# Kernel optimization log

Measured on AMD Instinct MI355X. Metric: run time of the kernel, lower is better.

Reference implementation:

```python
import jax, jax.numpy as jnp
import numpy as np

SHIFT = 1  # fixed shift_direction (original picks +-1 randomly at init)


def setup_inputs() -> dict:
    key = jax.random.key(0)
    kx, kw = jax.random.split(key)
    x = jax.random.normal(kx, (128, 256, 28, 28), dtype=jnp.float32)
    W = jax.random.normal(kw, (32, 3, 4, 3, 8), dtype=jnp.float32)
    return {"x": x, "W": W}


def reference(x, W):
    # (128,256,28,28) -> (128,2,128,28,28) -> sum over dim 1 -> (128,128,28,28)
    t = x.reshape(128, 2, 128, 28, 28).sum(axis=1)
    # split channels into 32 groups of 4: (n, i=32, m=4, h=28, w=28)
    t = t.reshape(128, 32, 4, 28, 28)
    # first unfold: kernel (3,1), pad (1,0) over the i=32 axis -> neighbor stack j in {-1,0,+1}
    tp = jnp.pad(t, ((0, 0), (1, 1), (0, 0), (0, 0), (0, 0)))
    t3 = jnp.stack([tp[:, 0:32], tp[:, 1:33], tp[:, 2:34]], axis=1)  # (n, j3, i32, m, h, w)
    # cyclic shift along w
    t3 = jnp.roll(t3, SHIFT, axis=5)
    # second unfold: kernel (3,1), pad (1,0) over the w axis -> neighbor stack kw in {-1,0,+1}
    tp2 = jnp.pad(t3, ((0, 0), (0, 0), (0, 0), (0, 0), (0, 0), (1, 1)))
    t3 = jnp.stack([tp2[..., 0:28], tp2[..., 1:29], tp2[..., 2:30]], axis=5)  # (n, j3, i32, m, h, kw, w)
    # contraction: einsum labels match torch 'njimpol,jimlk->njpok' after its permute.
    # Our t3 dims (n, i_e=3, j_e=32, m=4, p=h, l=kw, o=w); W dims (j=32, i=3, m=4, l=3, k=8)
    out = jnp.einsum('nijmplo,jimlk->njpok', t3, W)  # (128, 32, 28, 28, 8)
    out = out.transpose(0, 2, 3, 1, 4).reshape(128, 28, 28, 256)
    out = jnp.roll(out, SHIFT, axis=1)
    return out.transpose(0, 3, 1, 2)  # (128, 256, 28, 28)
```

## Files before the change

### kernel.cpp

```cpp
#include <hip/hip_runtime.h>

typedef float __attribute__((ext_vector_type(4))) f32x4;
typedef unsigned int u32;
typedef u32 __attribute__((ext_vector_type(4))) u32x4;


__device__ __forceinline__ u32 pack2bf(float lo, float hi) {
    u32 a = __float_as_uint(lo), b = __float_as_uint(hi);
    a = (a + 0x7FFFu + ((a >> 16) & 1u)) >> 16;
    b = (b + 0x7FFFu + ((b >> 16) & 1u)) >> 16;
    return a | (b << 16);
}

__device__ __forceinline__ float dot2bf(u32 t2, u32 w2, float acc) {
    asm("v_dot2_f32_bf16 %0, %1, %2, %0" : "+v"(acc) : "v"(t2), "v"(w2));
    return acc;
}

__global__ __launch_bounds__(256, 8) void fused_shift_conv(
    const float* __restrict__ x, const float* __restrict__ Wt, float* __restrict__ out)
{
    __shared__ __align__(16) u32 L[3840];

    const int tid  = threadIdx.x;
    const int blk  = blockIdx.x;
    const int half = blk & 1;
    const int rest = blk >> 1;
    const int n    = rest / 14;
    const int b2   = rest - n * 14;
    const int h0   = b2 * 2;
    const int J0   = half * 16;

    const float* xn = x + (size_t)n * 200704;

    #pragma unroll
    for (int it = 0; it < 2; ++it) {
        const int f = tid + it * 256;
        if (f < 504) {
            const int pl  = f / 14;
            const int rem = f - pl * 14;
            const int row = rem / 7;
            const int q   = rem - row * 7;
            const int gl  = pl >> 1;
            const int mp  = pl & 1;
            const int g   = J0 - 1 + gl;
            int hs = h0 - 1 + row;
            hs = hs < 0 ? 27 : hs;
            u32x4 wv = {0u, 0u, 0u, 0u};
            if (g >= 0 && g <= 31) {
                const int ch0 = g * 4 + mp * 2;
                const float* b0 = xn + ch0 * 784 + hs * 28 + q * 4;
                const f32x4 l0 = *(const f32x4*)b0;
                const f32x4 l1 = *(const f32x4*)(b0 + 784);
                const f32x4 u0 = *(const f32x4*)(b0 + 100352);
                const f32x4 u1 = *(const f32x4*)(b0 + 784 + 100352);
                const f32x4 s0 = l0 + u0, s1 = l1 + u1;
                #pragma unroll
                for (int e = 0; e < 4; ++e) wv[e] = pack2bf(s0[e], s1[e]);
            }
            const int sw = gl & 7;
            *(u32x4*)&L[row * 1152 + pl * 32 + ((q ^ sw) << 2)] = wv;
        }
    }

    const int tloc = tid & 127;
    const int s_   = tid >> 7;
    const int jl   = tloc >> 3;
    const int j    = J0 + jl;
    const int k    = tloc & 7;
    u32 w2[3][2][3];
    {
        const float* wp = Wt + j * 288 + k;
        #pragma unroll
        for (int a = 0; a < 3; ++a)
            #pragma unroll
            for (int m2 = 0; m2 < 2; ++m2)
                #pragma unroll
                for (int bb = 0; bb < 3; ++bb)
                    w2[a][m2][bb] = pack2bf(wp[a*96 + (2*m2  )*24 + bb*8],
                                            wp[a*96 + (2*m2+1)*24 + bb*8]);
    }
    if (j == 0) {
        #pragma unroll
        for (int m2 = 0; m2 < 2; ++m2)
            #pragma unroll
            for (int bb = 0; bb < 3; ++bb) w2[0][m2][bb] = 0u;
    }
    if (j == 31) {
        #pragma unroll
        for (int m2 = 0; m2 < 2; ++m2)
            #pragma unroll
            for (int bb = 0; bb < 3; ++bb) w2[2][m2][bb] = 0u;
    }

    int rb_c[4], rb_r[4];
    #pragma unroll
    for (int it = 0; it < 4; ++it) {
        const int fo = tid + it * 256;
        rb_c[it] = fo / 14;
        rb_r[it] = fo - rb_c[it] * 14;
    }

    __syncthreads();

    const u32* Bs = L + s_ * 1152;
    float acc[28];
    #pragma unroll
    for (int w = 0; w < 28; ++w) acc[w] = 0.f;

    #pragma unroll
    for (int a = 0; a < 3; ++a) {
        const int gl = jl + a;
        const int s  = gl & 7;
        #pragma unroll
        for (int m2 = 0; m2 < 2; ++m2) {
            const int rowd = (gl * 2 + m2) * 32;
            const u32 t2 = w2[a][m2][2], t1 = w2[a][m2][1], t0 = w2[a][m2][0];
            #pragma unroll
            for (int qb = 0; qb < 7; ++qb) {
                const u32x4 v = *(const u32x4*)&Bs[rowd + ((qb ^ s) << 2)];
                #pragma unroll
                for (int e = 0; e < 4; ++e) {
                    const int wp_ = qb * 4 + e;
                    if (wp_ != 27) acc[wp_] = dot2bf(v[e], t2, acc[wp_]);
                    acc[(wp_ + 1) % 28] = dot2bf(v[e], t1, acc[(wp_ + 1) % 28]);
                    if (wp_ != 26) acc[(wp_ + 2) % 28] = dot2bf(v[e], t0, acc[(wp_ + 2) % 28]);
                }
            }
        }
    }

    float* Lf = (float*)L;
    float* outb = out + (size_t)n * 200704 + (size_t)(J0 * 8) * 784 + h0 * 28;
    #pragma unroll
    for (int c = 0; c < 2; ++c) {
        __syncthreads();
        if ((tloc >> 6) == c) {
            float* dst = Lf + (tloc & 63) * 60 + s_ * 28;
            #pragma unroll
            for (int qq = 0; qq < 7; ++qq) {
                f32x4 o;
                o.x = acc[qq * 4 + 0];
                o.y = acc[qq * 4 + 1];
                o.z = acc[qq * 4 + 2];
                o.w = acc[qq * 4 + 3];
                *(f32x4*)(dst + qq * 4) = o;
            }
        }
        __syncthreads();
        float* outc = outb + (size_t)(c * 64) * 784;
        #pragma unroll
        for (int it = 0; it < 4; ++it) {
            if (tid + it * 256 < 896) {
                const f32x4 v = *(const f32x4*)(Lf + rb_c[it] * 60 + rb_r[it] * 4);
                *(f32x4*)(outc + (size_t)rb_c[it] * 784 + rb_r[it] * 4) = v;
            }
        }
    }
}

extern "C" void kernel_launch(void* const* d_in, const int* in_sizes, int n_in,
                              void* d_out, int out_size, void* d_ws, size_t ws_size,
                              hipStream_t stream) {
    const float* x  = (const float*)d_in[0];
    const float* Wt = (const float*)d_in[1];
    float* out      = (float*)d_out;

    const int nbatch = in_sizes[0] / 200704;
    fused_shift_conv<<<nbatch * 28, 256, 0, stream>>>(x, Wt, out);
}
```

Measured before the change: 50.37 us.

## Process four output rows per block with prefetch of next input rows

Each block now covers four output rows (two passes of two) instead of two, so the grid is halved. The weight packing and index setup are reused across both passes. The second pass's global loads are issued before the first pass's output store so they overlap it. Input and transpose staging now use separate shared buffers, which raises LDS use, and launch bounds drop to 6 blocks per CU, which may reduce occupancy.

```diff
diff --git a/kernel.cpp b/kernel.cpp
--- a/kernel.cpp
+++ b/kernel.cpp
@@ -17,97 +17,10 @@
     return acc;
 }
 
-__global__ __launch_bounds__(256, 8) void fused_shift_conv(
-    const float* __restrict__ x, const float* __restrict__ Wt, float* __restrict__ out)
-{
-    __shared__ __align__(16) u32 L[3840];
-
-    const int tid  = threadIdx.x;
-    const int blk  = blockIdx.x;
-    const int half = blk & 1;
-    const int rest = blk >> 1;
-    const int n    = rest / 14;
-    const int b2   = rest - n * 14;
-    const int h0   = b2 * 2;
-    const int J0   = half * 16;
-
-    const float* xn = x + (size_t)n * 200704;
-
-    #pragma unroll
-    for (int it = 0; it < 2; ++it) {
-        const int f = tid + it * 256;
-        if (f < 504) {
-            const int pl  = f / 14;
-            const int rem = f - pl * 14;
-            const int row = rem / 7;
-            const int q   = rem - row * 7;
-            const int gl  = pl >> 1;
-            const int mp  = pl & 1;
-            const int g   = J0 - 1 + gl;
-            int hs = h0 - 1 + row;
-            hs = hs < 0 ? 27 : hs;
-            u32x4 wv = {0u, 0u, 0u, 0u};
-            if (g >= 0 && g <= 31) {
-                const int ch0 = g * 4 + mp * 2;
-                const float* b0 = xn + ch0 * 784 + hs * 28 + q * 4;
-                const f32x4 l0 = *(const f32x4*)b0;
-                const f32x4 l1 = *(const f32x4*)(b0 + 784);
-                const f32x4 u0 = *(const f32x4*)(b0 + 100352);
-                const f32x4 u1 = *(const f32x4*)(b0 + 784 + 100352);
-                const f32x4 s0 = l0 + u0, s1 = l1 + u1;
-                #pragma unroll
-                for (int e = 0; e < 4; ++e) wv[e] = pack2bf(s0[e], s1[e]);
-            }
-            const int sw = gl & 7;
-            *(u32x4*)&L[row * 1152 + pl * 32 + ((q ^ sw) << 2)] = wv;
-        }
-    }
-
-    const int tloc = tid & 127;
-    const int s_   = tid >> 7;
-    const int jl   = tloc >> 3;
-    const int j    = J0 + jl;
-    const int k    = tloc & 7;
-    u32 w2[3][2][3];
-    {
-        const float* wp = Wt + j * 288 + k;
-        #pragma unroll
-        for (int a = 0; a < 3; ++a)
-            #pragma unroll
-            for (int m2 = 0; m2 < 2; ++m2)
-                #pragma unroll
-                for (int bb = 0; bb < 3; ++bb)
-                    w2[a][m2][bb] = pack2bf(wp[a*96 + (2*m2  )*24 + bb*8],
-                                            wp[a*96 + (2*m2+1)*24 + bb*8]);
-    }
-    if (j == 0) {
-        #pragma unroll
-        for (int m2 = 0; m2 < 2; ++m2)
-            #pragma unroll
-            for (int bb = 0; bb < 3; ++bb) w2[0][m2][bb] = 0u;
-    }
-    if (j == 31) {
-        #pragma unroll
-        for (int m2 = 0; m2 < 2; ++m2)
-            #pragma unroll
-            for (int bb = 0; bb < 3; ++bb) w2[2][m2][bb] = 0u;
-    }
-
-    int rb_c[4], rb_r[4];
-    #pragma unroll
-    for (int it = 0; it < 4; ++it) {
-        const int fo = tid + it * 256;
-        rb_c[it] = fo / 14;
-        rb_r[it] = fo - rb_c[it] * 14;
-    }
-
-    __syncthreads();
-
-    const u32* Bs = L + s_ * 1152;
-    float acc[28];
+__device__ __forceinline__ void compute_row(const u32* Bs, const u32 (*w2)[2][3],
+                                            int jl, float* acc) {
     #pragma unroll
     for (int w = 0; w < 28; ++w) acc[w] = 0.f;
-
     #pragma unroll
     for (int a = 0; a < 3; ++a) {
         const int gl = jl + a;
@@ -129,14 +42,16 @@
             }
         }
     }
-
-    float* Lf = (float*)L;
-    float* outb = out + (size_t)n * 200704 + (size_t)(J0 * 8) * 784 + h0 * 28;
+}
+
+__device__ __forceinline__ void tail_store(const float* acc, float* LT, float* outb,
+                                           int tid, int tloc, int s_,
+                                           const int* rb_c, const int* rb_r) {
     #pragma unroll
     for (int c = 0; c < 2; ++c) {
         __syncthreads();
         if ((tloc >> 6) == c) {
-            float* dst = Lf + (tloc & 63) * 60 + s_ * 28;
+            float* dst = LT + (tloc & 63) * 60 + s_ * 28;
             #pragma unroll
             for (int qq = 0; qq < 7; ++qq) {
                 f32x4 o;
@@ -152,11 +67,145 @@
         #pragma unroll
         for (int it = 0; it < 4; ++it) {
             if (tid + it * 256 < 896) {
-                const f32x4 v = *(const f32x4*)(Lf + rb_c[it] * 60 + rb_r[it] * 4);
+                const f32x4 v = *(const f32x4*)(LT + rb_c[it] * 60 + rb_r[it] * 4);
                 *(f32x4*)(outc + (size_t)rb_c[it] * 784 + rb_r[it] * 4) = v;
             }
         }
     }
+}
+
+__global__ __launch_bounds__(256, 6) void fused_shift_conv(
+    const float* __restrict__ x, const float* __restrict__ Wt, float* __restrict__ out)
+{
+    __shared__ __align__(16) u32   LIN[2304];
+    __shared__ __align__(16) float LT[3840];
+
+    const int tid  = threadIdx.x;
+    const int blk  = blockIdx.x;
+    const int half = blk & 1;
+    const int rest = blk >> 1;
+    const int n    = rest / 7;
+    const int q4   = rest - n * 7;
+    const int h0   = q4 * 4;
+    const int J0   = half * 16;
+
+    const float* xn = x + (size_t)n * 200704;
+
+    int ldso[2], chq[2], rowv[2];
+    bool val[2], okg[2];
+    #pragma unroll
+    for (int it = 0; it < 2; ++it) {
+        const int f = tid + it * 256;
+        val[it] = f < 504;
+        const int pl  = f / 14;
+        const int rem = f - pl * 14;
+        const int row = rem / 7;
+        const int q   = rem - row * 7;
+        const int gl  = pl >> 1;
+        const int mp  = pl & 1;
+        const int g   = J0 - 1 + gl;
+        rowv[it] = row;
+        okg[it]  = val[it] && g >= 0 && g <= 31;
+        chq[it]  = okg[it] ? ((g * 4 + mp * 2) * 784 + q * 4) : 0;
+        ldso[it] = row * 1152 + pl * 32 + ((q ^ (gl & 7)) << 2);
+    }
+
+    #pragma unroll
+    for (int it = 0; it < 2; ++it) {
+        if (val[it]) {
+            int hs = h0 - 1 + rowv[it]; if (hs < 0) hs = 27;
+            u32x4 wv = {0u, 0u, 0u, 0u};
+            if (okg[it]) {
+                const float* b0 = xn + chq[it] + hs * 28;
+                const f32x4 l0 = *(const f32x4*)b0;
+                const f32x4 l1 = *(const f32x4*)(b0 + 784);
+                const f32x4 u0 = *(const f32x4*)(b0 + 100352);
+                const f32x4 u1 = *(const f32x4*)(b0 + 100352 + 784);
+                const f32x4 s0 = l0 + u0, s1 = l1 + u1;
+                wv[0] = pack2bf(s0[0], s1[0]);
+                wv[1] = pack2bf(s0[1], s1[1]);
+                wv[2] = pack2bf(s0[2], s1[2]);
+                wv[3] = pack2bf(s0[3], s1[3]);
+            }
+            *(u32x4*)&LIN[ldso[it]] = wv;
+        }
+    }
+
+    const int tloc = tid & 127;
+    const int s_   = tid >> 7;
+    const int jl   = tloc >> 3;
+    const int j    = J0 + jl;
+    const int k    = tloc & 7;
+    u32 w2[3][2][3];
+    {
+        const float* wp = Wt + j * 288 + k;
+        #pragma unroll
+        for (int a = 0; a < 3; ++a)
+            #pragma unroll
+            for (int m2 = 0; m2 < 2; ++m2)
+                #pragma unroll
+                for (int bb = 0; bb < 3; ++bb)
+                    w2[a][m2][bb] = pack2bf(wp[a*96 + (2*m2  )*24 + bb*8],
+                                            wp[a*96 + (2*m2+1)*24 + bb*8]);
+    }
+    if (j == 0) {
+        #pragma unroll
+        for (int m2 = 0; m2 < 2; ++m2)
+            #pragma unroll
+            for (int bb = 0; bb < 3; ++bb) w2[0][m2][bb] = 0u;
+    }
+    if (j == 31) {
+        #pragma unroll
+        for (int m2 = 0; m2 < 2; ++m2)
+            #pragma unroll
+            for (int bb = 0; bb < 3; ++bb) w2[2][m2][bb] = 0u;
+    }
+
+    int rb_c[4], rb_r[4];
+    #pragma unroll
+    for (int it = 0; it < 4; ++it) {
+        const int fo = tid + it * 256;
+        rb_c[it] = fo / 14;
+        rb_r[it] = fo - rb_c[it] * 14;
+    }
+
+    __syncthreads();
+
+    float acc0[28];
+    compute_row(LIN + s_ * 1152, w2, jl, acc0);
+
+    f32x4 pfa[2], pfb[2];
+    #pragma unroll
+    for (int it = 0; it < 2; ++it) {
+        pfa[it] = (f32x4){0.f, 0.f, 0.f, 0.f};
+        pfb[it] = (f32x4){0.f, 0.f, 0.f, 0.f};
+        if (okg[it]) {
+            const int hs = h0 + 1 + rowv[it];
+            const float* b0 = xn + chq[it] + hs * 28;
+            pfa[it] = *(const f32x4*)b0         + *(const f32x4*)(b0 + 100352);
+            pfb[it] = *(const f32x4*)(b0 + 784) + *(const f32x4*)(b0 + 100352 + 784);
+        }
+    }
+
+    float* outb0 = out + (size_t)n * 200704 + (size_t)(J0 * 8) * 784 + h0 * 28;
+    tail_store(acc0, LT, outb0, tid, tloc, s_, rb_c, rb_r);
+
+    #pragma unroll
+    for (int it = 0; it < 2; ++it) {
+        if (val[it]) {
+            u32x4 wv;
+            wv[0] = pack2bf(pfa[it][0], pfb[it][0]);
+            wv[1] = pack2bf(pfa[it][1], pfb[it][1]);
+            wv[2] = pack2bf(pfa[it][2], pfb[it][2]);
+            wv[3] = pack2bf(pfa[it][3], pfb[it][3]);
+            *(u32x4*)&LIN[ldso[it]] = wv;
+        }
+    }
+    __syncthreads();
+
+    float acc1[28];
+    compute_row(LIN + s_ * 1152, w2, jl, acc1);
+    tail_store(acc1, LT, outb0 + 2 * 28, tid, tloc, s_, rb_c, rb_r);
 }
 
 extern "C" void kernel_launch(void* const* d_in, const int* in_sizes, int n_in,
@@ -167,5 +216,5 @@
     float* out      = (float*)d_out;
 
     const int nbatch = in_sizes[0] / 200704;
-    fused_shift_conv<<<nbatch * 28, 256, 0, stream>>>(x, Wt, out);
-}
+    fused_shift_conv<<<nbatch * 14, 256, 0, stream>>>(x, Wt, out);
+}
```

Measured after the change: 83.45 us. 1.66x slower.
